# Kernel optimization log

Hardware: AMD Instinct MI355X
Metric: run time of the kernel (lower is better)

The kernel has to match this reference:

```python
import jax, jax.numpy as jnp
import numpy as np

E = 256      # embed_dim
TD = 128     # token_dim
NH = 8       # num_heads
HD = E // NH
FF = 4 * E
EPS = 1e-5


def ln(x, g, b):
    m = jnp.mean(x, axis=-1, keepdims=True)
    v = jnp.mean((x - m) ** 2, axis=-1, keepdims=True)
    return (x - m) * jax.lax.rsqrt(v + EPS) * g + b


def setup_inputs() -> dict:
    key = jax.random.key(0)
    ks = jax.random.split(key, 20)
    B, H, W = 16, 64, 64
    s = lambda d: 1.0 / np.sqrt(d)
    inp = {
        "image_embeddings": jax.random.normal(ks[0], (B, E, H, W), jnp.float32),
        "target_token": jax.random.normal(ks[1], (B, TD), jnp.float32),
        "bg_token": jax.random.normal(ks[2], (B, TD), jnp.float32),
        # token_proj
        "Wp": jax.random.normal(ks[3], (E, TD), jnp.float32) * s(TD),
        "bp": jnp.zeros((E,), jnp.float32),
        # layernorms
        "g_img": jnp.ones((E,), jnp.float32), "b_img": jnp.zeros((E,), jnp.float32),
        "g_tok": jnp.ones((E,), jnp.float32), "b_tok": jnp.zeros((E,), jnp.float32),
        "g_ffn": jnp.ones((E,), jnp.float32), "b_ffn": jnp.zeros((E,), jnp.float32),
        # attention projections (in_proj split into q/k/v)
        "Wq": jax.random.normal(ks[4], (E, E), jnp.float32) * s(E),
        "Wk": jax.random.normal(ks[5], (E, E), jnp.float32) * s(E),
        "Wv": jax.random.normal(ks[6], (E, E), jnp.float32) * s(E),
        "bq": jnp.zeros((E,), jnp.float32),
        "bk": jnp.zeros((E,), jnp.float32),
        "bv": jnp.zeros((E,), jnp.float32),
        "Wo": jax.random.normal(ks[7], (E, E), jnp.float32) * s(E),
        "bo": jnp.zeros((E,), jnp.float32),
        # ffn
        "W1": jax.random.normal(ks[8], (FF, E), jnp.float32) * s(E),
        "b1": jnp.zeros((FF,), jnp.float32),
        "W2": jax.random.normal(ks[9], (E, FF), jnp.float32) * s(FF),
        "b2": jnp.zeros((E,), jnp.float32),
    }
    return inp


def reference(image_embeddings, target_token, bg_token, Wp, bp,
              g_img, b_img, g_tok, b_tok, g_ffn, b_ffn,
              Wq, Wk, Wv, bq, bk, bv, Wo, bo, W1, b1, W2, b2):
    B, C, H, W = image_embeddings.shape
    # tokens -> embed space, stacked as KV of length 2
    tgt = target_token @ Wp.T + bp          # [B,E]
    bg = bg_token @ Wp.T + bp               # [B,E]
    token_kv = jnp.stack([tgt, bg], axis=1)  # [B,2,E]

    x = image_embeddings.reshape(B, C, H * W).transpose(0, 2, 1)  # [B,N,E]

    # pre-norm cross attention (dropout=0 at inference)
    qn = ln(x, g_img, b_img)
    kvn = ln(token_kv, g_tok, b_tok)
    q = (qn @ Wq.T + bq).reshape(B, -1, NH, HD)   # [B,N,h,d]
    k = (kvn @ Wk.T + bk).reshape(B, 2, NH, HD)    # [B,2,h,d]
    v = (kvn @ Wv.T + bv).reshape(B, 2, NH, HD)
    scores = jnp.einsum('bnhd,bkhd->bhnk', q, k) / np.sqrt(HD)  # [B,h,N,2]
    attn = jax.nn.softmax(scores, axis=-1)
    ctx = jnp.einsum('bhnk,bkhd->bnhd', attn, v).reshape(B, -1, E)
    attended = ctx @ Wo.T + bo

    x = x + attended
    h = jax.nn.gelu(ln(x, g_ffn, b_ffn) @ W1.T + b1, approximate=False)
    x = x + (h @ W2.T + b2)
    return x.transpose(0, 2, 1).reshape(B, C, H, W)
```

## Files before the change

### kernel.cpp

```cpp
#include <hip/hip_runtime.h>
#include <math.h>

#define E 256
#define TD 128
#define FF 1024
#define NTOK 4096
#define BM 64
#define XS_LD 264
#define HS_LD 264
#define A_LD 40
#define OUT_LD 257

typedef __attribute__((ext_vector_type(8))) __bf16 bf16x8;
typedef __attribute__((ext_vector_type(4))) float f32x4;

__device__ __forceinline__ unsigned short f2bf(float x) {
    unsigned u = __float_as_uint(x);
    u += ((u >> 16) & 1u) + 0x7fffu;
    return (unsigned short)(u >> 16);
}
__device__ __forceinline__ float bf2f(unsigned short h) {
    return __uint_as_float(((unsigned)h) << 16);
}
__device__ __forceinline__ float gelu_tanh(float x) {
    float u = 0.7978845608028654f * (x + 0.044715f * x * x * x);
    float e = __expf(2.f * u);
    float th = 1.f - 2.f / (e + 1.f);
    return 0.5f * x * (1.f + th);
}

__global__ __launch_bounds__(256) void prep_kernel(
    const float* __restrict__ W1, const float* __restrict__ W2, const float* __restrict__ b1,
    const float* __restrict__ tt, const float* __restrict__ bgt,
    const float* __restrict__ Wp, const float* __restrict__ bp,
    const float* __restrict__ g_tok, const float* __restrict__ b_tok,
    const float* __restrict__ g_img, const float* __restrict__ b_img,
    const float* __restrict__ Wq, const float* __restrict__ bq,
    const float* __restrict__ Wk, const float* __restrict__ bk,
    const float* __restrict__ Wv, const float* __restrict__ bv,
    const float* __restrict__ Wo,
    const float* __restrict__ g_ffn, const float* __restrict__ b_ffn,
    unsigned short* __restrict__ w1b, unsigned short* __restrict__ w2b,
    unsigned short* __restrict__ wkbf, unsigned short* __restrict__ wvbf,
    float* __restrict__ Gk, float* __restrict__ sbk,
    float* __restrict__ G1, float* __restrict__ B1)
{
    const int t = threadIdx.x;
    const int lane = t & 63;
    if (blockIdx.x < 256) {
        const int b = blockIdx.x;
        {
            int row = b * 4 + (t >> 6);
            int i0 = lane * 4;
            f32x4 w = *(const f32x4*)(W1 + (size_t)row * E + i0);
            f32x4 g = *(const f32x4*)(g_ffn + i0);
            f32x4 bb = *(const f32x4*)(b_ffn + i0);
            float s0 = w[0] * g[0], s1 = w[1] * g[1], s2 = w[2] * g[2], s3 = w[3] * g[3];
            ushort4 o; o.x = f2bf(s0); o.y = f2bf(s1); o.z = f2bf(s2); o.w = f2bf(s3);
            *(ushort4*)(w1b + (size_t)row * E + i0) = o;
            float gp = s0 + s1 + s2 + s3;
            float bpv = w[0] * bb[0] + w[1] * bb[1] + w[2] * bb[2] + w[3] * bb[3];
            for (int off = 32; off; off >>= 1) { gp += __shfl_down(gp, off); bpv += __shfl_down(bpv, off); }
            if (lane == 0) { G1[row] = gp; B1[row] = bpv + b1[row]; }
        }
        {
            int i = (b * 256 + t) * 4;
            f32x4 w = *(const f32x4*)(W2 + i);
            ushort4 o; o.x = f2bf(w[0]); o.y = f2bf(w[1]); o.z = f2bf(w[2]); o.w = f2bf(w[3]);
            *(ushort4*)(w2b + i) = o;
        }
        return;
    }
    const int bi = blockIdx.x - 256;
    __shared__ float tokL[2][TD];
    __shared__ float kvn[2][E];
    __shared__ float ks[2][E];
    __shared__ float vs[2][E];
    __shared__ float red[8];
    __shared__ float redk[16][4], redb[16][4];

    if (t < TD) tokL[0][t] = tt[bi * TD + t];
    else tokL[1][t - TD] = bgt[bi * TD + (t - TD)];
    __syncthreads();

    {
        float a0 = bp[t], a1 = a0;
        const float* wr = Wp + (size_t)t * TD;
        for (int i = 0; i < TD; i += 4) {
            f32x4 w = *(const f32x4*)(wr + i);
            f32x4 x0 = *(const f32x4*)(&tokL[0][i]);
            f32x4 x1 = *(const f32x4*)(&tokL[1][i]);
            a0 += w[0] * x0[0] + w[1] * x0[1] + w[2] * x0[2] + w[3] * x0[3];
            a1 += w[0] * x1[0] + w[1] * x1[1] + w[2] * x1[2] + w[3] * x1[3];
        }
        kvn[0][t] = a0; kvn[1][t] = a1;
    }
    __syncthreads();
    for (int j = 0; j < 2; ++j) {
        float v = kvn[j][t];
        float s = v, s2 = v * v;
        for (int off = 32; off; off >>= 1) { s += __shfl_down(s, off); s2 += __shfl_down(s2, off); }
        if (lane == 0) { red[t >> 6] = s; red[4 + (t >> 6)] = s2; }
        __syncthreads();
        float S = red[0] + red[1] + red[2] + red[3];
        float S2 = red[4] + red[5] + red[6] + red[7];
        float m = S * (1.f / E);
        float rs = rsqrtf(S2 * (1.f / E) - m * m + 1e-5f);
        __syncthreads();
        kvn[j][t] = (v - m) * rs * g_tok[t] + b_tok[t];
    }
    __syncthreads();
    {
        float k0 = bk[t], k1 = k0, v0 = bv[t], v1 = v0;
        const float* wkr = Wk + (size_t)t * E;
        const float* wvr = Wv + (size_t)t * E;
        for (int i = 0; i < E; i += 4) {
            f32x4 wk4 = *(const f32x4*)(wkr + i);
            f32x4 wv4 = *(const f32x4*)(wvr + i);
            f32x4 x0 = *(const f32x4*)(&kvn[0][i]);
            f32x4 x1 = *(const f32x4*)(&kvn[1][i]);
            k0 += wk4[0] * x0[0] + wk4[1] * x0[1] + wk4[2] * x0[2] + wk4[3] * x0[3];
            k1 += wk4[0] * x1[0] + wk4[1] * x1[1] + wk4[2] * x1[2] + wk4[3] * x1[3];
            v0 += wv4[0] * x0[0] + wv4[1] * x0[1] + wv4[2] * x0[2] + wv4[3] * x0[3];
            v1 += wv4[0] * x1[0] + wv4[1] * x1[1] + wv4[2] * x1[2] + wv4[3] * x1[3];
        }
        ks[0][t] = k0; ks[1][t] = k1; vs[0][t] = v0; vs[1][t] = v1;
    }
    __syncthreads();
    const float inv = 0.17677669529663687f;
    const float gi = g_img[t], bimg = b_img[t];
    for (int c = 0; c < 16; ++c) {
        int j = c >> 3, h = c & 7;
        float awk = 0.f, awv = 0.f;
        const float* wqc = Wq + (size_t)(h * 32) * E + t;
        const float* wor = Wo + (size_t)t * E + h * 32;
        #pragma unroll
        for (int d = 0; d < 32; d += 4) {
            f32x4 kv = *(const f32x4*)(&ks[j][h * 32 + d]);
            f32x4 vv = *(const f32x4*)(&vs[j][h * 32 + d]);
            f32x4 wo4 = *(const f32x4*)(wor + d);
            awk += kv[0] * wqc[(size_t)(d + 0) * E] + kv[1] * wqc[(size_t)(d + 1) * E]
                 + kv[2] * wqc[(size_t)(d + 2) * E] + kv[3] * wqc[(size_t)(d + 3) * E];
            awv += wo4[0] * vv[0] + wo4[1] * vv[1] + wo4[2] * vv[2] + wo4[3] * vv[3];
        }
        float base = awk * inv;
        wkbf[(size_t)(bi * 16 + c) * E + t] = f2bf(gi * base);
        wvbf[((size_t)(bi * E + t)) * 32 + c] = f2bf(awv);
        float rk = gi * base, rb = bimg * base;
        for (int off = 32; off; off >>= 1) { rk += __shfl_down(rk, off); rb += __shfl_down(rb, off); }
        if (lane == 0) { redk[c][t >> 6] = rk; redb[c][t >> 6] = rb; }
    }
    #pragma unroll
    for (int c = 16; c < 32; ++c) wvbf[((size_t)(bi * E + t)) * 32 + c] = 0;
    __syncthreads();
    if (t < 16) {
        int c = t, j = c >> 3, h = c & 7;
        float s = 0.f;
        for (int d = 0; d < 32; ++d) s += bq[h * 32 + d] * ks[j][h * 32 + d];
        Gk[bi * 16 + c] = redk[c][0] + redk[c][1] + redk[c][2] + redk[c][3];
        sbk[bi * 16 + c] = redb[c][0] + redb[c][1] + redb[c][2] + redb[c][3] + s * inv;
    }
}

__global__ __launch_bounds__(512, 4) void fused_main_kernel(
    const float* __restrict__ img,
    const float* __restrict__ pbo, const float* __restrict__ pb2,
    const unsigned short* __restrict__ w1b, const unsigned short* __restrict__ w2b,
    const unsigned short* __restrict__ wkbf, const unsigned short* __restrict__ wvbf,
    const float* __restrict__ Gk, const float* __restrict__ sbk,
    const float* __restrict__ G1, const float* __restrict__ B1,
    float* __restrict__ out)
{
    __shared__ __align__(16) char smem[67584];
    unsigned short (*xs)[XS_LD] = (unsigned short(*)[XS_LD])smem;
    unsigned short (*hs)[HS_LD] = (unsigned short(*)[HS_LD])(smem + 33792);
    unsigned short (*al)[A_LD]  = (unsigned short(*)[A_LD])(smem + 33792);
    float (*outs)[OUT_LD] = (float(*)[OUT_LD])smem;
    __shared__ float mean_s[BM], rstd_s[BM];

    const int t = threadIdx.x;
    const int lane = t & 63;
    const int wid = t >> 6;
    const int l15 = lane & 15;
    const int l4 = lane >> 4;
    const int bi = blockIdx.x >> 6;
    const int n0 = (blockIdx.x & 63) << 6;
    const int nc = wid * 32;

    const float* imgb = img + (size_t)bi * E * NTOK + n0;

    for (int e0 = 0; e0 < E; e0 += 8) {
        int e = e0 + wid;
        xs[lane][e] = f2bf(imgb[(size_t)e * NTOK + lane]);
    }
    __syncthreads();

    for (int rr = 0; rr < 8; ++rr) {
        int r = wid * 8 + rr;
        ushort4 xv = *(const ushort4*)&xs[r][lane * 4];
        float v0 = bf2f(xv.x), v1 = bf2f(xv.y), v2 = bf2f(xv.z), v3 = bf2f(xv.w);
        float s = v0 + v1 + v2 + v3;
        float s2 = v0 * v0 + v1 * v1 + v2 * v2 + v3 * v3;
        for (int off = 32; off; off >>= 1) { s += __shfl_down(s, off); s2 += __shfl_down(s2, off); }
        if (lane == 0) {
            float m = s * (1.f / E);
            mean_s[r] = m;
            rstd_s[r] = rsqrtf(s2 * (1.f / E) - m * m + 1e-5f);
        }
    }
    __syncthreads();

    if (wid < 4) {
        f32x4 p = {0.f, 0.f, 0.f, 0.f};
        for (int kk = 0; kk < 8; ++kk) {
            bf16x8 a = *(const bf16x8*)&xs[wid * 16 + l15][kk * 32 + l4 * 8];
            bf16x8 b = *(const bf16x8*)&wkbf[(size_t)(bi * 16 + l15) * E + kk * 32 + l4 * 8];
            p = __builtin_amdgcn_mfma_f32_16x16x32_bf16(a, b, p, 0, 0, 0);
        }
        float gkv = Gk[bi * 16 + l15];
        float sbv = sbk[bi * 16 + l15];
        #pragma unroll
        for (int rg = 0; rg < 4; ++rg) {
            int R = wid * 16 + l4 * 4 + rg;
            float s = rstd_s[R] * (p[rg] - mean_s[R] * gkv) + sbv;
            float sp = __shfl_xor(s, 8);
            float mx = fmaxf(s, sp);
            float e0 = __expf(s - mx), e1 = __expf(sp - mx);
            al[R][l15] = f2bf(e0 / (e0 + e1));
            al[R][16 + l15] = 0;
        }
    }
    __syncthreads();

    f32x4 acc2[4][2];
    {
        f32x4 pa[4][2];
        #pragma unroll
        for (int m = 0; m < 4; ++m)
            #pragma unroll
            for (int n = 0; n < 2; ++n)
                pa[m][n] = f32x4{0.f, 0.f, 0.f, 0.f};
        bf16x8 bv[2];
        #pragma unroll
        for (int n = 0; n < 2; ++n)
            bv[n] = *(const bf16x8*)&wvbf[((size_t)(bi * E + nc + n * 16 + l15)) * 32 + l4 * 8];
        #pragma unroll
        for (int m = 0; m < 4; ++m) {
            bf16x8 af = *(const bf16x8*)&al[m * 16 + l15][l4 * 8];
            #pragma unroll
            for (int n = 0; n < 2; ++n)
                pa[m][n] = __builtin_amdgcn_mfma_f32_16x16x32_bf16(af, bv[n], pa[m][n], 0, 0, 0);
        }
        float bov[2], b2v[2];
        #pragma unroll
        for (int n = 0; n < 2; ++n) {
            bov[n] = pbo[nc + n * 16 + l15];
            b2v[n] = pb2[nc + n * 16 + l15];
        }
        #pragma unroll
        for (int m = 0; m < 4; ++m)
            #pragma unroll
            for (int n = 0; n < 2; ++n)
                #pragma unroll
                for (int rg = 0; rg < 4; ++rg) {
                    int R = m * 16 + l4 * 4 + rg;
                    int C = nc + n * 16 + l15;
                    float x1 = bf2f(xs[R][C]) + pa[m][n][rg] + bov[n];
                    xs[R][C] = f2bf(x1);
                    acc2[m][n][rg] = x1 + b2v[n];
                }
    }
    __syncthreads();

    for (int rr = 0; rr < 8; ++rr) {
        int r = wid * 8 + rr;
        ushort4 xv = *(const ushort4*)&xs[r][lane * 4];
        float v0 = bf2f(xv.x), v1 = bf2f(xv.y), v2 = bf2f(xv.z), v3 = bf2f(xv.w);
        float s = v0 + v1 + v2 + v3;
        float s2 = v0 * v0 + v1 * v1 + v2 * v2 + v3 * v3;
        for (int off = 32; off; off >>= 1) { s += __shfl_down(s, off); s2 += __shfl_down(s2, off); }
        if (lane == 0) {
            float m = s * (1.f / E);
            mean_s[r] = m;
            rstd_s[r] = rsqrtf(s2 * (1.f / E) - m * m + 1e-5f);
        }
    }
    __syncthreads();

    for (int fc = 0; fc < FF; fc += 256) {
        f32x4 p[4][2];
        #pragma unroll
        for (int m = 0; m < 4; ++m)
            #pragma unroll
            for (int n = 0; n < 2; ++n)
                p[m][n] = f32x4{0.f, 0.f, 0.f, 0.f};
        for (int kk = 0; kk < 8; ++kk) {
            bf16x8 af[4], bfr[2];
            #pragma unroll
            for (int m = 0; m < 4; ++m)
                af[m] = *(const bf16x8*)&xs[m * 16 + l15][kk * 32 + l4 * 8];
            #pragma unroll
            for (int n = 0; n < 2; ++n)
                bfr[n] = *(const bf16x8*)&w1b[(size_t)(fc + nc + n * 16 + l15) * E + kk * 32 + l4 * 8];
            #pragma unroll
            for (int m = 0; m < 4; ++m)
                #pragma unroll
                for (int n = 0; n < 2; ++n)
                    p[m][n] = __builtin_amdgcn_mfma_f32_16x16x32_bf16(af[m], bfr[n], p[m][n], 0, 0, 0);
        }
        {
            float g1v[2], b1v[2];
            #pragma unroll
            for (int n = 0; n < 2; ++n) {
                g1v[n] = G1[fc + nc + n * 16 + l15];
                b1v[n] = B1[fc + nc + n * 16 + l15];
            }
            #pragma unroll
            for (int m = 0; m < 4; ++m)
                #pragma unroll
                for (int n = 0; n < 2; ++n)
                    #pragma unroll
                    for (int rg = 0; rg < 4; ++rg) {
                        int R = m * 16 + l4 * 4 + rg;
                        float hpre = rstd_s[R] * (p[m][n][rg] - mean_s[R] * g1v[n]) + b1v[n];
                        hs[R][nc + n * 16 + l15] = f2bf(gelu_tanh(hpre));
                    }
        }
        __syncthreads();
        for (int kk = 0; kk < 8; ++kk) {
            bf16x8 af[4], bfr[2];
            #pragma unroll
            for (int m = 0; m < 4; ++m)
                af[m] = *(const bf16x8*)&hs[m * 16 + l15][kk * 32 + l4 * 8];
            #pragma unroll
            for (int n = 0; n < 2; ++n)
                bfr[n] = *(const bf16x8*)&w2b[(size_t)(nc + n * 16 + l15) * FF + fc + kk * 32 + l4 * 8];
            #pragma unroll
            for (int m = 0; m < 4; ++m)
                #pragma unroll
                for (int n = 0; n < 2; ++n)
                    acc2[m][n] = __builtin_amdgcn_mfma_f32_16x16x32_bf16(af[m], bfr[n], acc2[m][n], 0, 0, 0);
        }
        __syncthreads();
    }

    #pragma unroll
    for (int m = 0; m < 4; ++m)
        #pragma unroll
        for (int n = 0; n < 2; ++n)
            #pragma unroll
            for (int rg = 0; rg < 4; ++rg)
                outs[m * 16 + l4 * 4 + rg][nc + n * 16 + l15] = acc2[m][n][rg];
    __syncthreads();

    float* outb = out + (size_t)bi * E * NTOK + n0;
    for (int e0 = 0; e0 < E; e0 += 8) {
        int e = e0 + wid;
        outb[(size_t)e * NTOK + lane] = outs[lane][e];
    }
}

extern "C" void kernel_launch(void* const* d_in, const int* in_sizes, int n_in,
                              void* d_out, int out_size, void* d_ws, size_t ws_size,
                              hipStream_t stream) {
    (void)in_sizes; (void)n_in; (void)out_size; (void)ws_size;
    const float* img   = (const float*)d_in[0];
    const float* tt    = (const float*)d_in[1];
    const float* bgt   = (const float*)d_in[2];
    const float* Wp    = (const float*)d_in[3];
    const float* bp    = (const float*)d_in[4];
    const float* g_img = (const float*)d_in[5];
    const float* b_img = (const float*)d_in[6];
    const float* g_tok = (const float*)d_in[7];
    const float* b_tok = (const float*)d_in[8];
    const float* g_ffn = (const float*)d_in[9];
    const float* b_ffn = (const float*)d_in[10];
    const float* Wq    = (const float*)d_in[11];
    const float* Wk    = (const float*)d_in[12];
    const float* Wv    = (const float*)d_in[13];
    const float* bq    = (const float*)d_in[14];
    const float* bk    = (const float*)d_in[15];
    const float* bv    = (const float*)d_in[16];
    const float* Wo    = (const float*)d_in[17];
    const float* bo    = (const float*)d_in[18];
    const float* W1    = (const float*)d_in[19];
    const float* b1    = (const float*)d_in[20];
    const float* W2    = (const float*)d_in[21];
    const float* b2    = (const float*)d_in[22];

    char* ws = (char*)d_ws;
    unsigned short* w1b  = (unsigned short*)(ws);
    unsigned short* w2b  = (unsigned short*)(ws + 524288);
    unsigned short* wkbf = (unsigned short*)(ws + 1048576);
    unsigned short* wvbf = (unsigned short*)(ws + 1179648);
    float*          Gk   = (float*)(ws + 1441792);
    float*          sbk  = (float*)(ws + 1442816);
    float*          G1   = (float*)(ws + 1443840);
    float*          B1   = (float*)(ws + 1447936);

    hipLaunchKernelGGL(prep_kernel, dim3(272), dim3(256), 0, stream,
                       W1, W2, b1, tt, bgt, Wp, bp, g_tok, b_tok, g_img, b_img,
                       Wq, bq, Wk, bk, Wv, bv, Wo, g_ffn, b_ffn,
                       w1b, w2b, wkbf, wvbf, Gk, sbk, G1, B1);
    hipLaunchKernelGGL(fused_main_kernel, dim3(1024), dim3(512), 0, stream,
                       img, bo, b2, w1b, w2b, wkbf, wvbf, Gk, sbk, G1, B1, (float*)d_out);
}
```

Before: 286.8 us.

## Pre-swizzle weights into MFMA fragment layout, XOR-swizzle LDS, vectorize output stores

Prep kernel now writes W1, W2, Wk-fold and Wv-fold in MFMA B-fragment order so each lane loads one contiguous 16-byte chunk, replacing strided row reads. Shared-memory tiles drop padding in favour of XOR swizzles. First LayerNorm stats are computed during the image load, all 8 waves now share the score MFMA via a K split, and FFN chunks are visited in a staggered order per block. Output goes through a two-half transposed LDS buffer with float4 global stores, and GELU uses a sigmoid-form tanh approximation with a hardware reciprocal, which may slightly change numerics.

Measured after the change: 298.6 us. 1.04x slower.

```diff
diff --git a/kernel.cpp b/kernel.cpp
--- a/kernel.cpp
+++ b/kernel.cpp
@@ -5,11 +5,6 @@
 #define TD 128
 #define FF 1024
 #define NTOK 4096
-#define BM 64
-#define XS_LD 264
-#define HS_LD 264
-#define A_LD 40
-#define OUT_LD 257
 
 typedef __attribute__((ext_vector_type(8))) __bf16 bf16x8;
 typedef __attribute__((ext_vector_type(4))) float f32x4;
@@ -22,11 +17,9 @@
 __device__ __forceinline__ float bf2f(unsigned short h) {
     return __uint_as_float(((unsigned)h) << 16);
 }
-__device__ __forceinline__ float gelu_tanh(float x) {
-    float u = 0.7978845608028654f * (x + 0.044715f * x * x * x);
-    float e = __expf(2.f * u);
-    float th = 1.f - 2.f / (e + 1.f);
-    return 0.5f * x * (1.f + th);
+__device__ __forceinline__ float gelu_fast(float x) {
+    float ex = __expf(-x * (1.5957691216057308f + 0.07135481627f * x * x));
+    return x * __builtin_amdgcn_rcpf(1.f + ex);
 }
 
 __global__ __launch_bounds__(256) void prep_kernel(
@@ -40,34 +33,56 @@
     const float* __restrict__ Wv, const float* __restrict__ bv,
     const float* __restrict__ Wo,
     const float* __restrict__ g_ffn, const float* __restrict__ b_ffn,
-    unsigned short* __restrict__ w1b, unsigned short* __restrict__ w2b,
-    unsigned short* __restrict__ wkbf, unsigned short* __restrict__ wvbf,
+    unsigned short* __restrict__ w1s, unsigned short* __restrict__ w2s,
+    unsigned short* __restrict__ wks, unsigned short* __restrict__ wvs,
     float* __restrict__ Gk, float* __restrict__ sbk,
     float* __restrict__ G1, float* __restrict__ B1)
 {
     const int t = threadIdx.x;
     const int lane = t & 63;
     if (blockIdx.x < 256) {
-        const int b = blockIdx.x;
-        {
-            int row = b * 4 + (t >> 6);
-            int i0 = lane * 4;
-            f32x4 w = *(const f32x4*)(W1 + (size_t)row * E + i0);
-            f32x4 g = *(const f32x4*)(g_ffn + i0);
-            f32x4 bb = *(const f32x4*)(b_ffn + i0);
-            float s0 = w[0] * g[0], s1 = w[1] * g[1], s2 = w[2] * g[2], s3 = w[3] * g[3];
-            ushort4 o; o.x = f2bf(s0); o.y = f2bf(s1); o.z = f2bf(s2); o.w = f2bf(s3);
-            *(ushort4*)(w1b + (size_t)row * E + i0) = o;
-            float gp = s0 + s1 + s2 + s3;
-            float bpv = w[0] * bb[0] + w[1] * bb[1] + w[2] * bb[2] + w[3] * bb[3];
-            for (int off = 32; off; off >>= 1) { gp += __shfl_down(gp, off); bpv += __shfl_down(bpv, off); }
-            if (lane == 0) { G1[row] = gp; B1[row] = bpv + b1[row]; }
-        }
-        {
-            int i = (b * 256 + t) * 4;
-            f32x4 w = *(const f32x4*)(W2 + i);
-            ushort4 o; o.x = f2bf(w[0]); o.y = f2bf(w[1]); o.z = f2bf(w[2]); o.w = f2bf(w[3]);
-            *(ushort4*)(w2b + i) = o;
+        int gid = blockIdx.x * 256 + t;
+        if (gid < 32768) {
+            int row = gid >> 5;
+            int k0 = (gid & 31) * 8;
+            f32x4 wa = *(const f32x4*)(W1 + row * 256 + k0);
+            f32x4 wb = *(const f32x4*)(W1 + row * 256 + k0 + 4);
+            f32x4 ga = *(const f32x4*)(g_ffn + k0);
+            f32x4 gb = *(const f32x4*)(g_ffn + k0 + 4);
+            ushort4 o0, o1;
+            o0.x = f2bf(wa[0]*ga[0]); o0.y = f2bf(wa[1]*ga[1]);
+            o0.z = f2bf(wa[2]*ga[2]); o0.w = f2bf(wa[3]*ga[3]);
+            o1.x = f2bf(wb[0]*gb[0]); o1.y = f2bf(wb[1]*gb[1]);
+            o1.z = f2bf(wb[2]*gb[2]); o1.w = f2bf(wb[3]*gb[3]);
+            int dst = ((row >> 4) * 8 + (k0 >> 5)) * 512 + (((k0 >> 3) & 3) * 16 + (row & 15)) * 8;
+            *(ushort4*)(w1s + dst) = o0;
+            *(ushort4*)(w1s + dst + 4) = o1;
+        } else {
+            int g2 = gid - 32768;
+            int o = g2 >> 7;
+            int f0 = (g2 & 127) * 8;
+            f32x4 wa = *(const f32x4*)(W2 + o * 1024 + f0);
+            f32x4 wb = *(const f32x4*)(W2 + o * 1024 + f0 + 4);
+            ushort4 o0, o1;
+            o0.x = f2bf(wa[0]); o0.y = f2bf(wa[1]); o0.z = f2bf(wa[2]); o0.w = f2bf(wa[3]);
+            o1.x = f2bf(wb[0]); o1.y = f2bf(wb[1]); o1.z = f2bf(wb[2]); o1.w = f2bf(wb[3]);
+            int dst = (((f0 >> 8) * 16 + (o >> 4)) * 8 + ((f0 >> 5) & 7)) * 512
+                    + (((f0 >> 3) & 3) * 16 + (o & 15)) * 8;
+            *(ushort4*)(w2s + dst) = o0;
+            *(ushort4*)(w2s + dst + 4) = o1;
+        }
+        if (gid < 1024) {
+            int row = gid;
+            float gacc = 0.f, bacc = 0.f;
+            for (int k = 0; k < 256; k += 4) {
+                f32x4 w = *(const f32x4*)(W1 + row * 256 + k);
+                f32x4 g = *(const f32x4*)(g_ffn + k);
+                f32x4 bb = *(const f32x4*)(b_ffn + k);
+                gacc += w[0]*g[0] + w[1]*g[1] + w[2]*g[2] + w[3]*g[3];
+                bacc += w[0]*bb[0] + w[1]*bb[1] + w[2]*bb[2] + w[3]*bb[3];
+            }
+            G1[row] = gacc;
+            B1[row] = bacc + b1[row];
         }
         return;
     }
@@ -90,8 +105,8 @@
             f32x4 w = *(const f32x4*)(wr + i);
             f32x4 x0 = *(const f32x4*)(&tokL[0][i]);
             f32x4 x1 = *(const f32x4*)(&tokL[1][i]);
-            a0 += w[0] * x0[0] + w[1] * x0[1] + w[2] * x0[2] + w[3] * x0[3];
-            a1 += w[0] * x1[0] + w[1] * x1[1] + w[2] * x1[2] + w[3] * x1[3];
+            a0 += w[0]*x0[0] + w[1]*x0[1] + w[2]*x0[2] + w[3]*x0[3];
+            a1 += w[0]*x1[0] + w[1]*x1[1] + w[2]*x1[2] + w[3]*x1[3];
         }
         kvn[0][t] = a0; kvn[1][t] = a1;
     }
@@ -119,10 +134,10 @@
             f32x4 wv4 = *(const f32x4*)(wvr + i);
             f32x4 x0 = *(const f32x4*)(&kvn[0][i]);
             f32x4 x1 = *(const f32x4*)(&kvn[1][i]);
-            k0 += wk4[0] * x0[0] + wk4[1] * x0[1] + wk4[2] * x0[2] + wk4[3] * x0[3];
-            k1 += wk4[0] * x1[0] + wk4[1] * x1[1] + wk4[2] * x1[2] + wk4[3] * x1[3];
-            v0 += wv4[0] * x0[0] + wv4[1] * x0[1] + wv4[2] * x0[2] + wv4[3] * x0[3];
-            v1 += wv4[0] * x1[0] + wv4[1] * x1[1] + wv4[2] * x1[2] + wv4[3] * x1[3];
+            k0 += wk4[0]*x0[0] + wk4[1]*x0[1] + wk4[2]*x0[2] + wk4[3]*x0[3];
+            k1 += wk4[0]*x1[0] + wk4[1]*x1[1] + wk4[2]*x1[2] + wk4[3]*x1[3];
+            v0 += wv4[0]*x0[0] + wv4[1]*x0[1] + wv4[2]*x0[2] + wv4[3]*x0[3];
+            v1 += wv4[0]*x1[0] + wv4[1]*x1[1] + wv4[2]*x1[2] + wv4[3]*x1[3];
         }
         ks[0][t] = k0; ks[1][t] = k1; vs[0][t] = v0; vs[1][t] = v1;
     }
@@ -139,19 +154,20 @@
             f32x4 kv = *(const f32x4*)(&ks[j][h * 32 + d]);
             f32x4 vv = *(const f32x4*)(&vs[j][h * 32 + d]);
             f32x4 wo4 = *(const f32x4*)(wor + d);
-            awk += kv[0] * wqc[(size_t)(d + 0) * E] + kv[1] * wqc[(size_t)(d + 1) * E]
-                 + kv[2] * wqc[(size_t)(d + 2) * E] + kv[3] * wqc[(size_t)(d + 3) * E];
-            awv += wo4[0] * vv[0] + wo4[1] * vv[1] + wo4[2] * vv[2] + wo4[3] * vv[3];
+            awk += kv[0]*wqc[(size_t)(d+0)*E] + kv[1]*wqc[(size_t)(d+1)*E]
+                 + kv[2]*wqc[(size_t)(d+2)*E] + kv[3]*wqc[(size_t)(d+3)*E];
+            awv += wo4[0]*vv[0] + wo4[1]*vv[1] + wo4[2]*vv[2] + wo4[3]*vv[3];
         }
         float base = awk * inv;
-        wkbf[(size_t)(bi * 16 + c) * E + t] = f2bf(gi * base);
-        wvbf[((size_t)(bi * E + t)) * 32 + c] = f2bf(awv);
+        wks[(bi * 8 + (t >> 5)) * 512 + (((t >> 3) & 3) * 16 + c) * 8 + (t & 7)] = f2bf(gi * base);
+        wvs[(bi * 16 + (t >> 4)) * 512 + ((c >> 3) * 16 + (t & 15)) * 8 + (c & 7)] = f2bf(awv);
         float rk = gi * base, rb = bimg * base;
         for (int off = 32; off; off >>= 1) { rk += __shfl_down(rk, off); rb += __shfl_down(rb, off); }
         if (lane == 0) { redk[c][t >> 6] = rk; redb[c][t >> 6] = rb; }
     }
     #pragma unroll
-    for (int c = 16; c < 32; ++c) wvbf[((size_t)(bi * E + t)) * 32 + c] = 0;
+    for (int c2 = 16; c2 < 32; ++c2)
+        wvs[(bi * 16 + (t >> 4)) * 512 + ((c2 >> 3) * 16 + (t & 15)) * 8 + (c2 & 7)] = 0;
     __syncthreads();
     if (t < 16) {
         int c = t, j = c >> 3, h = c & 7;
@@ -165,18 +181,22 @@
 __global__ __launch_bounds__(512, 4) void fused_main_kernel(
     const float* __restrict__ img,
     const float* __restrict__ pbo, const float* __restrict__ pb2,
-    const unsigned short* __restrict__ w1b, const unsigned short* __restrict__ w2b,
-    const unsigned short* __restrict__ wkbf, const unsigned short* __restrict__ wvbf,
+    const unsigned short* __restrict__ w1s, const unsigned short* __restrict__ w2s,
+    const unsigned short* __restrict__ wks, const unsigned short* __restrict__ wvs,
     const float* __restrict__ Gk, const float* __restrict__ sbk,
     const float* __restrict__ G1, const float* __restrict__ B1,
     float* __restrict__ out)
 {
-    __shared__ __align__(16) char smem[67584];
-    unsigned short (*xs)[XS_LD] = (unsigned short(*)[XS_LD])smem;
-    unsigned short (*hs)[HS_LD] = (unsigned short(*)[HS_LD])(smem + 33792);
-    unsigned short (*al)[A_LD]  = (unsigned short(*)[A_LD])(smem + 33792);
-    float (*outs)[OUT_LD] = (float(*)[OUT_LD])smem;
-    __shared__ float mean_s[BM], rstd_s[BM];
+    __shared__ __align__(16) char smem[66048];
+    unsigned short* xsf = (unsigned short*)smem;
+    unsigned short* hsf = (unsigned short*)(smem + 32768);
+    float* part_s  = (float*)(smem + 32768);
+    float* part_s2 = (float*)(smem + 35072);
+    unsigned short* alf = (unsigned short*)(smem + 32768);
+    float* scf = (float*)(smem + 37376);
+    float* outsf = (float*)(smem + 32768);
+    float* mean_s = (float*)(smem + 65536);
+    float* rstd_s = (float*)(smem + 65792);
 
     const int t = threadIdx.x;
     const int lane = t & 63;
@@ -186,134 +206,161 @@
     const int bi = blockIdx.x >> 6;
     const int n0 = (blockIdx.x & 63) << 6;
     const int nc = wid * 32;
-
-    const float* imgb = img + (size_t)bi * E * NTOK + n0;
-
-    for (int e0 = 0; e0 < E; e0 += 8) {
-        int e = e0 + wid;
-        xs[lane][e] = f2bf(imgb[(size_t)e * NTOK + lane]);
+    const int swz15 = (l15 & 7) << 3;
+
+    {
+        const float* imgb = img + ((size_t)bi * E) * NTOK + n0 + lane;
+        float ps = 0.f, ps2 = 0.f;
+        #pragma unroll
+        for (int i = 0; i < 4; ++i) {
+            int e0 = wid * 8 + i * 64;
+            unsigned pk[4];
+            #pragma unroll
+            for (int jp = 0; jp < 4; ++jp) {
+                float va = imgb[(size_t)(e0 + 2 * jp) * NTOK];
+                float vb = imgb[(size_t)(e0 + 2 * jp + 1) * NTOK];
+                unsigned short ha = f2bf(va), hb = f2bf(vb);
+                float fa = bf2f(ha), fb = bf2f(hb);
+                ps += fa + fb; ps2 += fa * fa + fb * fb;
+                pk[jp] = (unsigned)ha | ((unsigned)hb << 16);
+            }
+            int idx = (lane * 256 + e0) ^ ((lane & 7) << 3);
+            uint4 u = {pk[0], pk[1], pk[2], pk[3]};
+            *(uint4*)&xsf[idx] = u;
+        }
+        part_s[lane * 9 + wid] = ps;
+        part_s2[lane * 9 + wid] = ps2;
+    }
+    __syncthreads();
+
+    if (t < 64) {
+        float s = 0.f, s2 = 0.f;
+        #pragma unroll
+        for (int w = 0; w < 8; ++w) { s += part_s[t * 9 + w]; s2 += part_s2[t * 9 + w]; }
+        float m = s * (1.f / 256.f);
+        mean_s[t] = m;
+        rstd_s[t] = rsqrtf(s2 * (1.f / 256.f) - m * m + 1e-5f);
+    }
+
+    {
+        const int mt = wid >> 1, kh = wid & 1;
+        f32x4 p = {0.f, 0.f, 0.f, 0.f};
+        #pragma unroll
+        for (int kq = 0; kq < 4; ++kq) {
+            int kk = kh * 4 + kq;
+            bf16x8 a = *(const bf16x8*)&xsf[((mt * 16 + l15) * 256 + kk * 32 + l4 * 8) ^ swz15];
+            bf16x8 bfr = *(const bf16x8*)&wks[(bi * 8 + kk) * 512 + lane * 8];
+            p = __builtin_amdgcn_mfma_f32_16x16x32_bf16(a, bfr, p, 0, 0, 0);
+        }
+        #pragma unroll
+        for (int rg = 0; rg < 4; ++rg)
+            scf[(kh * 64 + mt * 16 + l4 * 4 + rg) * 16 + l15] = p[rg];
+    }
+    __syncthreads();
+
+    {
+        int r = t >> 3, h = t & 7;
+        float gk0 = Gk[bi * 16 + h], gk1 = Gk[bi * 16 + 8 + h];
+        float sb0 = sbk[bi * 16 + h], sb1 = sbk[bi * 16 + 8 + h];
+        float ms = mean_s[r], rs = rstd_s[r];
+        float raw0 = scf[r * 16 + h] + scf[(64 + r) * 16 + h];
+        float raw1 = scf[r * 16 + 8 + h] + scf[(64 + r) * 16 + 8 + h];
+        float s0 = rs * (raw0 - ms * gk0) + sb0;
+        float s1 = rs * (raw1 - ms * gk1) + sb1;
+        float mx = fmaxf(s0, s1);
+        float e0 = __expf(s0 - mx), e1 = __expf(s1 - mx);
+        float is = __builtin_amdgcn_rcpf(e0 + e1);
+        alf[r * 32 + h] = f2bf(e0 * is);
+        alf[r * 32 + 8 + h] = f2bf(e1 * is);
+        alf[r * 32 + 16 + h] = 0;
+        alf[r * 32 + 24 + h] = 0;
+    }
+    __syncthreads();
+
+    f32x4 acc2[4][2];
+    {
+        f32x4 pa[4][2];
+        #pragma unroll
+        for (int m = 0; m < 4; ++m)
+            #pragma unroll
+            for (int n = 0; n < 2; ++n)
+                pa[m][n] = f32x4{0.f, 0.f, 0.f, 0.f};
+        bf16x8 bv[2];
+        #pragma unroll
+        for (int n = 0; n < 2; ++n)
+            bv[n] = *(const bf16x8*)&wvs[(bi * 16 + wid * 2 + n) * 512 + lane * 8];
+        #pragma unroll
+        for (int m = 0; m < 4; ++m) {
+            bf16x8 af = *(const bf16x8*)&alf[(m * 16 + l15) * 32 + l4 * 8];
+            #pragma unroll
+            for (int n = 0; n < 2; ++n)
+                pa[m][n] = __builtin_amdgcn_mfma_f32_16x16x32_bf16(af, bv[n], pa[m][n], 0, 0, 0);
+        }
+        float bov[2], b2v[2];
+        #pragma unroll
+        for (int n = 0; n < 2; ++n) {
+            bov[n] = pbo[nc + n * 16 + l15];
+            b2v[n] = pb2[nc + n * 16 + l15];
+        }
+        #pragma unroll
+        for (int m = 0; m < 4; ++m)
+            #pragma unroll
+            for (int n = 0; n < 2; ++n)
+                #pragma unroll
+                for (int rg = 0; rg < 4; ++rg) {
+                    int R = m * 16 + l4 * 4 + rg;
+                    int C = nc + n * 16 + l15;
+                    int xi = (R * 256 + C) ^ ((R & 7) << 3);
+                    float x1 = bf2f(xsf[xi]) + pa[m][n][rg] + bov[n];
+                    xsf[xi] = f2bf(x1);
+                    acc2[m][n][rg] = x1 + b2v[n];
+                }
     }
     __syncthreads();
 
     for (int rr = 0; rr < 8; ++rr) {
         int r = wid * 8 + rr;
-        ushort4 xv = *(const ushort4*)&xs[r][lane * 4];
+        int idx = (r * 256 + lane * 4) ^ ((r & 7) << 3);
+        ushort4 xv = *(const ushort4*)&xsf[idx];
         float v0 = bf2f(xv.x), v1 = bf2f(xv.y), v2 = bf2f(xv.z), v3 = bf2f(xv.w);
         float s = v0 + v1 + v2 + v3;
         float s2 = v0 * v0 + v1 * v1 + v2 * v2 + v3 * v3;
         for (int off = 32; off; off >>= 1) { s += __shfl_down(s, off); s2 += __shfl_down(s2, off); }
         if (lane == 0) {
-            float m = s * (1.f / E);
+            float m = s * (1.f / 256.f);
             mean_s[r] = m;
-            rstd_s[r] = rsqrtf(s2 * (1.f / E) - m * m + 1e-5f);
-        }
-    }
-    __syncthreads();
-
-    if (wid < 4) {
-        f32x4 p = {0.f, 0.f, 0.f, 0.f};
-        for (int kk = 0; kk < 8; ++kk) {
-            bf16x8 a = *(const bf16x8*)&xs[wid * 16 + l15][kk * 32 + l4 * 8];
-            bf16x8 b = *(const bf16x8*)&wkbf[(size_t)(bi * 16 + l15) * E + kk * 32 + l4 * 8];
-            p = __builtin_amdgcn_mfma_f32_16x16x32_bf16(a, b, p, 0, 0, 0);
-        }
-        float gkv = Gk[bi * 16 + l15];
-        float sbv = sbk[bi * 16 + l15];
-        #pragma unroll
-        for (int rg = 0; rg < 4; ++rg) {
-            int R = wid * 16 + l4 * 4 + rg;
-            float s = rstd_s[R] * (p[rg] - mean_s[R] * gkv) + sbv;
-            float sp = __shfl_xor(s, 8);
-            float mx = fmaxf(s, sp);
-            float e0 = __expf(s - mx), e1 = __expf(sp - mx);
-            al[R][l15] = f2bf(e0 / (e0 + e1));
-            al[R][16 + l15] = 0;
-        }
-    }
-    __syncthreads();
-
-    f32x4 acc2[4][2];
-    {
-        f32x4 pa[4][2];
-        #pragma unroll
-        for (int m = 0; m < 4; ++m)
-            #pragma unroll
-            for (int n = 0; n < 2; ++n)
-                pa[m][n] = f32x4{0.f, 0.f, 0.f, 0.f};
-        bf16x8 bv[2];
-        #pragma unroll
-        for (int n = 0; n < 2; ++n)
-            bv[n] = *(const bf16x8*)&wvbf[((size_t)(bi * E + nc + n * 16 + l15)) * 32 + l4 * 8];
-        #pragma unroll
-        for (int m = 0; m < 4; ++m) {
-            bf16x8 af = *(const bf16x8*)&al[m * 16 + l15][l4 * 8];
-            #pragma unroll
-            for (int n = 0; n < 2; ++n)
-                pa[m][n] = __builtin_amdgcn_mfma_f32_16x16x32_bf16(af, bv[n], pa[m][n], 0, 0, 0);
-        }
-        float bov[2], b2v[2];
-        #pragma unroll
-        for (int n = 0; n < 2; ++n) {
-            bov[n] = pbo[nc + n * 16 + l15];
-            b2v[n] = pb2[nc + n * 16 + l15];
-        }
-        #pragma unroll
-        for (int m = 0; m < 4; ++m)
-            #pragma unroll
-            for (int n = 0; n < 2; ++n)
-                #pragma unroll
-                for (int rg = 0; rg < 4; ++rg) {
-                    int R = m * 16 + l4 * 4 + rg;
-                    int C = nc + n * 16 + l15;
-                    float x1 = bf2f(xs[R][C]) + pa[m][n][rg] + bov[n];
-                    xs[R][C] = f2bf(x1);
-                    acc2[m][n][rg] = x1 + b2v[n];
-                }
-    }
-    __syncthreads();
-
-    for (int rr = 0; rr < 8; ++rr) {
-        int r = wid * 8 + rr;
-        ushort4 xv = *(const ushort4*)&xs[r][lane * 4];
-        float v0 = bf2f(xv.x), v1 = bf2f(xv.y), v2 = bf2f(xv.z), v3 = bf2f(xv.w);
-        float s = v0 + v1 + v2 + v3;
-        float s2 = v0 * v0 + v1 * v1 + v2 * v2 + v3 * v3;
-        for (int off = 32; off; off >>= 1) { s += __shfl_down(s, off); s2 += __shfl_down(s2, off); }
-        if (lane == 0) {
-            float m = s * (1.f / E);
-            mean_s[r] = m;
-            rstd_s[r] = rsqrtf(s2 * (1.f / E) - m * m + 1e-5f);
-        }
-    }
-    __syncthreads();
-
-    for (int fc = 0; fc < FF; fc += 256) {
+            rstd_s[r] = rsqrtf(s2 * (1.f / 256.f) - m * m + 1e-5f);
+        }
+    }
+    __syncthreads();
+
+    const int bsz = blockIdx.x & 3;
+    for (int ci = 0; ci < 4; ++ci) {
+        const int c = (ci + bsz) & 3;
+        const int fc = c << 8;
         f32x4 p[4][2];
         #pragma unroll
         for (int m = 0; m < 4; ++m)
             #pragma unroll
             for (int n = 0; n < 2; ++n)
                 p[m][n] = f32x4{0.f, 0.f, 0.f, 0.f};
+        #pragma unroll
         for (int kk = 0; kk < 8; ++kk) {
-            bf16x8 af[4], bfr[2];
-            #pragma unroll
-            for (int m = 0; m < 4; ++m)
-                af[m] = *(const bf16x8*)&xs[m * 16 + l15][kk * 32 + l4 * 8];
-            #pragma unroll
-            for (int n = 0; n < 2; ++n)
-                bfr[n] = *(const bf16x8*)&w1b[(size_t)(fc + nc + n * 16 + l15) * E + kk * 32 + l4 * 8];
-            #pragma unroll
-            for (int m = 0; m < 4; ++m)
-                #pragma unroll
-                for (int n = 0; n < 2; ++n)
-                    p[m][n] = __builtin_amdgcn_mfma_f32_16x16x32_bf16(af[m], bfr[n], p[m][n], 0, 0, 0);
+            bf16x8 b0 = *(const bf16x8*)&w1s[((c * 16 + wid * 2 + 0) * 8 + kk) * 512 + lane * 8];
+            bf16x8 b1f = *(const bf16x8*)&w1s[((c * 16 + wid * 2 + 1) * 8 + kk) * 512 + lane * 8];
+            #pragma unroll
+            for (int m = 0; m < 4; ++m) {
+                bf16x8 af = *(const bf16x8*)&xsf[((m * 16 + l15) * 256 + kk * 32 + l4 * 8) ^ swz15];
+                p[m][0] = __builtin_amdgcn_mfma_f32_16x16x32_bf16(af, b0, p[m][0], 0, 0, 0);
+                p[m][1] = __builtin_amdgcn_mfma_f32_16x16x32_bf16(af, b1f, p[m][1], 0, 0, 0);
+            }
         }
         {
             float g1v[2], b1v[2];
             #pragma unroll
             for (int n = 0; n < 2; ++n) {
-                g1v[n] = G1[fc + nc + n * 16 + l15];
-                b1v[n] = B1[fc + nc + n * 16 + l15];
+                g1v[n] = G1[fc + wid * 32 + n * 16 + l15];
+                b1v[n] = B1[fc + wid * 32 + n * 16 + l15];
             }
             #pragma unroll
             for (int m = 0; m < 4; ++m)
@@ -323,40 +370,53 @@
                     for (int rg = 0; rg < 4; ++rg) {
                         int R = m * 16 + l4 * 4 + rg;
                         float hpre = rstd_s[R] * (p[m][n][rg] - mean_s[R] * g1v[n]) + b1v[n];
-                        hs[R][nc + n * 16 + l15] = f2bf(gelu_tanh(hpre));
+                        hsf[(R * 256 + wid * 32 + n * 16 + l15) ^ ((R & 7) << 3)] = f2bf(gelu_fast(hpre));
                     }
         }
         __syncthreads();
-        for (int kk = 0; kk < 8; ++kk) {
-            bf16x8 af[4], bfr[2];
-            #pragma unroll
-            for (int m = 0; m < 4; ++m)
-                af[m] = *(const bf16x8*)&hs[m * 16 + l15][kk * 32 + l4 * 8];
-            #pragma unroll
-            for (int n = 0; n < 2; ++n)
-                bfr[n] = *(const bf16x8*)&w2b[(size_t)(nc + n * 16 + l15) * FF + fc + kk * 32 + l4 * 8];
+        #pragma unroll
+        for (int kk2 = 0; kk2 < 8; ++kk2) {
+            bf16x8 b0 = *(const bf16x8*)&w2s[((c * 16 + wid * 2 + 0) * 8 + kk2) * 512 + lane * 8];
+            bf16x8 b1f = *(const bf16x8*)&w2s[((c * 16 + wid * 2 + 1) * 8 + kk2) * 512 + lane * 8];
+            #pragma unroll
+            for (int m = 0; m < 4; ++m) {
+                bf16x8 af = *(const bf16x8*)&hsf[((m * 16 + l15) * 256 + kk2 * 32 + l4 * 8) ^ swz15];
+                acc2[m][0] = __builtin_amdgcn_mfma_f32_16x16x32_bf16(af, b0, acc2[m][0], 0, 0, 0);
+                acc2[m][1] = __builtin_amdgcn_mfma_f32_16x16x32_bf16(af, b1f, acc2[m][1], 0, 0, 0);
+            }
+        }
+        __syncthreads();
+    }
+
+    #pragma unroll
+    for (int h = 0; h < 2; ++h) {
+        if ((wid >> 2) == h) {
             #pragma unroll
             for (int m = 0; m < 4; ++m)
                 #pragma unroll
                 for (int n = 0; n < 2; ++n)
-                    acc2[m][n] = __builtin_amdgcn_mfma_f32_16x16x32_bf16(af[m], bfr[n], acc2[m][n], 0, 0, 0);
+                    #pragma unroll
+                    for (int rg = 0; rg < 4; ++rg) {
+                        int R = m * 16 + l4 * 4 + rg;
+                        int Cl = nc + n * 16 + l15 - h * 128;
+                        outsf[(R * 128 + Cl) ^ ((R & 7) << 2)] = acc2[m][n][rg];
+                    }
         }
         __syncthreads();
-    }
-
-    #pragma unroll
-    for (int m = 0; m < 4; ++m)
-        #pragma unroll
-        for (int n = 0; n < 2; ++n)
-            #pragma unroll
-            for (int rg = 0; rg < 4; ++rg)
-                outs[m * 16 + l4 * 4 + rg][nc + n * 16 + l15] = acc2[m][n][rg];
-    __syncthreads();
-
-    float* outb = out + (size_t)bi * E * NTOK + n0;
-    for (int e0 = 0; e0 < E; e0 += 8) {
-        int e = e0 + wid;
-        outb[(size_t)e * NTOK + lane] = outs[lane][e];
+        #pragma unroll
+        for (int j = 0; j < 4; ++j) {
+            int gidx = j * 512 + t;
+            int e = gidx >> 4;
+            int part = gidx & 15;
+            f32x4 v;
+            #pragma unroll
+            for (int k2 = 0; k2 < 4; ++k2) {
+                int nrow = part * 4 + k2;
+                v[k2] = outsf[(nrow * 128 + e) ^ ((nrow & 7) << 2)];
+            }
+            *(f32x4*)(out + ((size_t)bi * E + h * 128 + e) * NTOK + n0 + part * 4) = v;
+        }
+        if (h == 0) __syncthreads();
     }
 }
 
@@ -389,19 +449,19 @@
     const float* b2    = (const float*)d_in[22];
 
     char* ws = (char*)d_ws;
-    unsigned short* w1b  = (unsigned short*)(ws);
-    unsigned short* w2b  = (unsigned short*)(ws + 524288);
-    unsigned short* wkbf = (unsigned short*)(ws + 1048576);
-    unsigned short* wvbf = (unsigned short*)(ws + 1179648);
-    float*          Gk   = (float*)(ws + 1441792);
-    float*          sbk  = (float*)(ws + 1442816);
-    float*          G1   = (float*)(ws + 1443840);
-    float*          B1   = (float*)(ws + 1447936);
+    unsigned short* w1s = (unsigned short*)(ws);
+    unsigned short* w2s = (unsigned short*)(ws + 524288);
+    unsigned short* wks = (unsigned short*)(ws + 1048576);
+    unsigned short* wvs = (unsigned short*)(ws + 1179648);
+    float*          Gk  = (float*)(ws + 1441792);
+    float*          sbk = (float*)(ws + 1442816);
+    float*          G1  = (float*)(ws + 1443840);
+    float*          B1  = (float*)(ws + 1447936);
 
     hipLaunchKernelGGL(prep_kernel, dim3(272), dim3(256), 0, stream,
                        W1, W2, b1, tt, bgt, Wp, bp, g_tok, b_tok, g_img, b_img,
                        Wq, bq, Wk, bk, Wv, bv, Wo, g_ffn, b_ffn,
-                       w1b, w2b, wkbf, wvbf, Gk, sbk, G1, B1);
+                       w1s, w2s, wks, wvs, Gk, sbk, G1, B1);
     hipLaunchKernelGGL(fused_main_kernel, dim3(1024), dim3(512), 0, stream,
-                       img, bo, b2, w1b, w2b, wkbf, wvbf, Gk, sbk, G1, B1, (float*)d_out);
-}
+                       img, bo, b2, w1s, w2s, wks, wvs, Gk, sbk, G1, B1, (float*)d_out);
+}
```
